# Kernel optimization log

Measured on AMD Instinct MI355X. Metric: run time of the kernel, lower is better.

## Reference

```python
import jax, jax.numpy as jnp
import numpy as np

N_NODES = 128   # input_series_dim (nodes per graph)
FEAT = 512      # input_series_length
HID = 512       # hidden_channels
OUT = 10        # output_dimension
BATCH = 512     # batch_size


def setup_inputs() -> dict:
    key = jax.random.key(0)
    ks = jax.random.split(key, 9)
    s = 0.02
    x = jax.random.normal(ks[0], (BATCH, N_NODES, FEAT), jnp.float32)
    # dense_to_sparse(ones(N_NODES, N_NODES)) -> fully connected incl. diagonal,
    # row-major order, covering only nodes 0..N_NODES-1 (faithful to source).
    r = jnp.repeat(jnp.arange(N_NODES, dtype=jnp.int32), N_NODES)
    c = jnp.tile(jnp.arange(N_NODES, dtype=jnp.int32), N_NODES)
    edge_index = jnp.stack([r, c])  # (2, N_NODES**2)
    batch = jnp.repeat(jnp.arange(BATCH, dtype=jnp.int32), N_NODES)  # (BATCH*N_NODES,)
    W1 = jax.random.normal(ks[1], (FEAT, HID), jnp.float32) * s
    b1 = jnp.zeros((HID,), jnp.float32)
    W2 = jax.random.normal(ks[2], (HID, HID), jnp.float32) * s
    b2 = jnp.zeros((HID,), jnp.float32)
    W3 = jax.random.normal(ks[3], (HID, HID), jnp.float32) * s
    b3 = jnp.zeros((HID,), jnp.float32)
    Wlin = jax.random.normal(ks[4], (HID, OUT), jnp.float32) * s
    blin = jnp.zeros((OUT,), jnp.float32)
    return {"x": x, "W1": W1, "b1": b1, "W2": W2, "b2": b2, "W3": W3,
            "b3": b3, "Wlin": Wlin, "blin": blin,
            "edge_index": edge_index, "batch": batch}


def gcn_conv(h, src, dst, W, b):
    # PyG GCNConv: linear transform, add self-loops for ALL N nodes, symmetric norm,
    # scatter-add aggregate at dst, add bias.
    N = h.shape[0]
    h = h @ W
    loop = jnp.arange(N, dtype=src.dtype)
    s = jnp.concatenate([src, loop])
    d = jnp.concatenate([dst, loop])
    deg = jax.ops.segment_sum(jnp.ones(s.shape[0], h.dtype), d, num_segments=N)
    dinv = jnp.where(deg > 0, jax.lax.rsqrt(deg), jnp.zeros((), h.dtype))
    norm = dinv[s] * dinv[d]                     # (E+N,)
    out = jax.ops.segment_sum(norm[:, None] * h[s], d, num_segments=N)
    return out + b


def reference(x, W1, b1, W2, b2, W3, b3, Wlin, blin, edge_index, batch):
    x = x.reshape(-1, x.shape[-1]).astype(jnp.float32)   # (B*N_NODES, FEAT)
    src, dst = edge_index[0], edge_index[1]
    h = jax.nn.relu(gcn_conv(x, src, dst, W1, b1))
    h = jax.nn.relu(gcn_conv(h, src, dst, W2, b2))
    h = gcn_conv(h, src, dst, W3, b3)                    # layers == 3 path
    B = BATCH
    sums = jax.ops.segment_sum(h, batch, num_segments=B)
    cnt = jax.ops.segment_sum(jnp.ones((h.shape[0],), h.dtype), batch, num_segments=B)
    pooled = sums / cnt[:, None]                         # global_mean_pool
    # dropout p=0.5 is identity in eval mode
    return pooled @ Wlin + blin                          # (BATCH, OUT)
```

## Files before the change

kernel.cpp:

```cpp
#include <hip/hip_runtime.h>
#include <hip/hip_bf16.h>


typedef __attribute__((ext_vector_type(8))) short short8;
typedef __attribute__((ext_vector_type(4))) float f32x4;
typedef __attribute__((ext_vector_type(2))) unsigned int uint2v;

#define AS_G __attribute__((address_space(1)))
#define AS_L __attribute__((address_space(3)))

__device__ __forceinline__ void gload_lds16(const void* g, void* l) {
  __builtin_amdgcn_global_load_lds((const AS_G void*)g, (AS_L void*)l, 16, 0, 0);
}

__device__ __forceinline__ unsigned int pack2_bf16(float a, float b) {
  unsigned int ua = __float_as_uint(a);
  unsigned int ub = __float_as_uint(b);
  ua += 0x7FFFu + ((ua >> 16) & 1u);
  ub += 0x7FFFu + ((ub >> 16) & 1u);
  return (ua >> 16) | (ub & 0xFFFF0000u);
}

__device__ __forceinline__ unsigned short bf16_rne(float a) {
  unsigned int ua = __float_as_uint(a);
  ua += 0x7FFFu + ((ua >> 16) & 1u);
  return (unsigned short)(ua >> 16);
}

__global__ __launch_bounds__(1024) void fused_gcn(
    const float* __restrict__ x,
    const __hip_bfloat16* __restrict__ W1t,
    const __hip_bfloat16* __restrict__ W2t,
    const float* __restrict__ b1,
    const float* __restrict__ b2,
    const float* __restrict__ Wf,
    const float* __restrict__ bfv,
    float* __restrict__ out)
{
  __shared__ __align__(16) __hip_bfloat16 smem[81920];

  const int t  = threadIdx.x;
  const int g  = blockIdx.x;
  const int wave = t >> 6;
  const int l    = t & 63;
  const int q    = l >> 4;
  const int r16  = l & 15;
  const int wm   = (wave & 1) * 64;
  const int wn   = (wave >> 1) * 64;

  const int arow = t >> 3;
  const int kq   = t & 7;
  const float* ga = x + ((size_t)g * 128 + arow) * 512 + kq * 4;
  const int awoff = arow * 32 + (((kq >> 1) ^ ((arow >> 1) & 3)) << 3) + (kq & 1) * 4;

  const int brow = t >> 2;
  const int bgc  = (t & 3) ^ ((brow >> 1) & 3);
  const size_t boff = (size_t)brow * 512 + bgc * 8;
  const __hip_bfloat16* g1b0 = W1t + boff;
  const __hip_bfloat16* g1b1 = g1b0 + (size_t)256 * 512;

  f32x4 acc[4][4];
#pragma unroll
  for (int i = 0; i < 4; ++i)
#pragma unroll
    for (int j = 0; j < 4; ++j)
      acc[i][j] = (f32x4)0.0f;

  {
    f32x4 a0 = *(const f32x4*)(const void*)ga;
    gload_lds16(g1b0, smem + 49152 + wave * 512);
    gload_lds16(g1b1, smem + 49152 + 8192 + wave * 512);
    uint2v w;
    w[0] = pack2_bf16(a0[0], a0[1]);
    w[1] = pack2_bf16(a0[2], a0[3]);
    *(uint2v*)(void*)(smem + awoff) = w;
  }
  for (int kt = 0; kt < 16; ++kt) {
    const int cur = kt & 1;
    const int nxt = cur ^ 1;
    __syncthreads();

    f32x4 aN;
    if (kt < 15) {
      const int ko = (kt + 1) * 32;
      aN = *(const f32x4*)(const void*)(ga + ko);
      gload_lds16(g1b0 + ko, smem + 49152 + nxt * 16384 + wave * 512);
      gload_lds16(g1b1 + ko, smem + 49152 + nxt * 16384 + 8192 + wave * 512);
    }

    short8 af[4], bfr[4];
#pragma unroll
    for (int i = 0; i < 4; ++i) {
      const int row = wm + i * 16 + r16;
      const int c   = (q ^ ((row >> 1) & 3)) << 3;
      af[i] = *(const short8*)(const void*)(smem + cur * 4096 + row * 32 + c);
    }
#pragma unroll
    for (int j = 0; j < 4; ++j) {
      const int row = wn + j * 16 + r16;
      const int c   = (q ^ ((row >> 1) & 3)) << 3;
      bfr[j] = *(const short8*)(const void*)(smem + 49152 + cur * 16384 + row * 32 + c);
    }
#pragma unroll
    for (int i = 0; i < 4; ++i)
#pragma unroll
      for (int j = 0; j < 4; ++j)
        acc[i][j] = __builtin_amdgcn_mfma_f32_16x16x32_bf16(af[i], bfr[j], acc[i][j], 0, 0, 0);

    if (kt < 15) {
      uint2v w;
      w[0] = pack2_bf16(aN[0], aN[1]);
      w[1] = pack2_bf16(aN[2], aN[3]);
      *(uint2v*)(void*)(smem + nxt * 4096 + awoff) = w;
    }
  }
  __syncthreads();

  const __hip_bfloat16* g2b0 = W2t + boff;
  const __hip_bfloat16* g2b1 = g2b0 + (size_t)256 * 512;
  gload_lds16(g2b0, smem + 65536 + wave * 512);

  float* redf = (float*)(smem + 73728);
  float* Sbuf = (float*)(smem + 75776);

  if (g == 0) {
    float sj[4];
#pragma unroll
    for (int j = 0; j < 4; ++j) {
      float a = 0.0f;
#pragma unroll
      for (int i = 0; i < 4; ++i)
#pragma unroll
        for (int r = 0; r < 4; ++r)
          a += acc[i][j][r];
      a += __shfl_xor(a, 16, 64);
      a += __shfl_xor(a, 32, 64);
      sj[j] = a;
    }
    if (q == 0) {
#pragma unroll
      for (int j = 0; j < 4; ++j) redf[wave * 64 + j * 16 + r16] = sj[j];
    }
    __syncthreads();
    if (t < 512)
      Sbuf[t] = redf[((t >> 6) * 2) * 64 + (t & 63)] +
                redf[((t >> 6) * 2 + 1) * 64 + (t & 63)];
    __syncthreads();
#pragma unroll
    for (int j = 0; j < 4; ++j) {
      const int col = wn + j * 16 + r16;
      const float bv = b1[col];
      const float Sv = Sbuf[col];
#pragma unroll
      for (int i = 0; i < 4; ++i)
#pragma unroll
        for (int r = 0; r < 4; ++r) {
          const int row = wm + i * 16 + q * 4 + r;
          const float v = fmaxf((Sv + acc[i][j][r]) * (1.0f / 129.0f) + bv, 0.0f);
          const float o = __shfl_xor(v, 1, 64);
          if ((r16 & 1) == 0) {
            const int sl = (col >> 3) ^ (row & 7);
            *(unsigned int*)(void*)(smem + row * 512 + sl * 8 + (col & 7)) = pack2_bf16(v, o);
          }
        }
    }
  } else {
#pragma unroll
    for (int j = 0; j < 4; ++j) {
      const int col = wn + j * 16 + r16;
      const float bv = b1[col];
#pragma unroll
      for (int i = 0; i < 4; ++i)
#pragma unroll
        for (int r = 0; r < 4; ++r) {
          const int row = wm + i * 16 + q * 4 + r;
          const float v = fmaxf(acc[i][j][r] + bv, 0.0f);
          const float o = __shfl_xor(v, 1, 64);
          if ((r16 & 1) == 0) {
            const int sl = (col >> 3) ^ (row & 7);
            *(unsigned int*)(void*)(smem + row * 512 + sl * 8 + (col & 7)) = pack2_bf16(v, o);
          }
        }
    }
  }

#pragma unroll
  for (int i = 0; i < 4; ++i)
#pragma unroll
    for (int j = 0; j < 4; ++j)
      acc[i][j] = (f32x4)0.0f;

  for (int kt = 0; kt < 16; ++kt) {
    __syncthreads();
    gload_lds16(g2b1 + kt * 32, smem + 73728 + wave * 512);
    if (wave < 8) {
      short8 af[4], bfr[4];
#pragma unroll
      for (int i = 0; i < 4; ++i) {
        const int row = wm + i * 16 + r16;
        const int sl  = (kt * 4 + q) ^ (row & 7);
        af[i] = *(const short8*)(const void*)(smem + row * 512 + sl * 8);
      }
#pragma unroll
      for (int j = 0; j < 4; ++j) {
        const int row = wn + j * 16 + r16;
        const int c   = (q ^ ((row >> 1) & 3)) << 3;
        bfr[j] = *(const short8*)(const void*)(smem + 65536 + row * 32 + c);
      }
      __builtin_amdgcn_s_setprio(1);
#pragma unroll
      for (int i = 0; i < 4; ++i)
#pragma unroll
        for (int j = 0; j < 4; ++j)
          acc[i][j] = __builtin_amdgcn_mfma_f32_16x16x32_bf16(af[i], bfr[j], acc[i][j], 0, 0, 0);
      __builtin_amdgcn_s_setprio(0);
    }
    __syncthreads();
    if (kt < 15)
      gload_lds16(g2b0 + (kt + 1) * 32, smem + 65536 + wave * 512);
    if (wave >= 8) {
      short8 af[4], bfr[4];
#pragma unroll
      for (int i = 0; i < 4; ++i) {
        const int row = wm + i * 16 + r16;
        const int sl  = (kt * 4 + q) ^ (row & 7);
        af[i] = *(const short8*)(const void*)(smem + row * 512 + sl * 8);
      }
#pragma unroll
      for (int j = 0; j < 4; ++j) {
        const int row = wn + j * 16 + r16;
        const int c   = (q ^ ((row >> 1) & 3)) << 3;
        bfr[j] = *(const short8*)(const void*)(smem + 65536 + row * 32 + c);
      }
      __builtin_amdgcn_s_setprio(1);
#pragma unroll
      for (int i = 0; i < 4; ++i)
#pragma unroll
        for (int j = 0; j < 4; ++j)
          acc[i][j] = __builtin_amdgcn_mfma_f32_16x16x32_bf16(af[i], bfr[j], acc[i][j], 0, 0, 0);
      __builtin_amdgcn_s_setprio(0);
    }
  }
  __syncthreads();

  float pj[4];
  if (g == 0) {
    float sj[4];
#pragma unroll
    for (int j = 0; j < 4; ++j) {
      float a = 0.0f;
#pragma unroll
      for (int i = 0; i < 4; ++i)
#pragma unroll
        for (int r = 0; r < 4; ++r)
          a += acc[i][j][r];
      a += __shfl_xor(a, 16, 64);
      a += __shfl_xor(a, 32, 64);
      sj[j] = a;
    }
    if (q == 0) {
#pragma unroll
      for (int j = 0; j < 4; ++j) redf[wave * 64 + j * 16 + r16] = sj[j];
    }
    __syncthreads();
    if (t < 512)
      Sbuf[t] = redf[((t >> 6) * 2) * 64 + (t & 63)] +
                redf[((t >> 6) * 2 + 1) * 64 + (t & 63)];
    __syncthreads();
#pragma unroll
    for (int j = 0; j < 4; ++j) {
      const float bv = b2[wn + j * 16 + r16];
      const float Sv = Sbuf[wn + j * 16 + r16];
      float a = 0.0f;
#pragma unroll
      for (int i = 0; i < 4; ++i)
#pragma unroll
        for (int r = 0; r < 4; ++r)
          a += fmaxf((Sv + acc[i][j][r]) * (1.0f / 129.0f) + bv, 0.0f);
      a += __shfl_xor(a, 16, 64);
      a += __shfl_xor(a, 32, 64);
      pj[j] = a;
    }
  } else {
#pragma unroll
    for (int j = 0; j < 4; ++j) {
      const float bv = b2[wn + j * 16 + r16];
      float a = 0.0f;
#pragma unroll
      for (int i = 0; i < 4; ++i)
#pragma unroll
        for (int r = 0; r < 4; ++r)
          a += fmaxf(acc[i][j][r] + bv, 0.0f);
      a += __shfl_xor(a, 16, 64);
      a += __shfl_xor(a, 32, 64);
      pj[j] = a;
    }
  }
  if (q == 0) {
#pragma unroll
    for (int j = 0; j < 4; ++j) redf[wave * 64 + j * 16 + r16] = pj[j];
  }
  __syncthreads();
  if (t < 512)
    Sbuf[t] =
        (redf[((t >> 6) * 2) * 64 + (t & 63)] +
         redf[((t >> 6) * 2 + 1) * 64 + (t & 63)]) * (1.0f / 128.0f);
  __syncthreads();

  if (wave < 10) {
    float s = 0.0f;
    for (int c = l; c < 512; c += 64) s += Sbuf[c] * Wf[c * 10 + wave];
#pragma unroll
    for (int off = 32; off; off >>= 1) s += __shfl_down(s, off, 64);
    if (l == 0) out[(size_t)g * 10 + wave] = s + bfv[wave];
  }
}

__global__ __launch_bounds__(1024) void prep(
    const float* __restrict__ W1, const float* __restrict__ W2,
    unsigned short* __restrict__ W1t, unsigned short* __restrict__ W2t,
    const float* __restrict__ W3, const float* __restrict__ Wlin,
    const float* __restrict__ b3, const float* __restrict__ blin,
    float* __restrict__ Wf, float* __restrict__ bfv) {
  const int b = blockIdx.x;
  if (b < 512) {
    __shared__ float tile[32][33];
    const int z  = b >> 8;
    const int by = (b >> 4) & 15;
    const int bx = b & 15;
    const float* W = z ? W2 : W1;
    unsigned short* Wt = z ? W2t : W1t;
    const int tx = threadIdx.x & 31;
    const int ty = threadIdx.x >> 5;
    tile[ty][tx] = W[(by * 32 + ty) * 512 + bx * 32 + tx];
    __syncthreads();
    Wt[(bx * 32 + ty) * 512 + by * 32 + tx] = bf16_rne(tile[tx][ty]);
  } else {
    const int c = b - 512;
    const int l = threadIdx.x;
    if (l < 64) {
      float acc[10];
#pragma unroll
      for (int o = 0; o < 10; ++o) acc[o] = 0.0f;
      for (int n = l; n < 512; n += 64) {
        const float wv = W3[c * 512 + n];
#pragma unroll
        for (int o = 0; o < 10; ++o) acc[o] += wv * Wlin[n * 10 + o];
      }
#pragma unroll
      for (int off = 32; off; off >>= 1)
#pragma unroll
        for (int o = 0; o < 10; ++o) acc[o] += __shfl_down(acc[o], off, 64);
      if (l == 0) {
#pragma unroll
        for (int o = 0; o < 10; ++o) Wf[c * 10 + o] = acc[o];
      }
      if (c < 10) {
        float s = 0.0f;
        for (int k = l; k < 512; k += 64) s += b3[k] * Wlin[k * 10 + c];
#pragma unroll
        for (int off = 32; off; off >>= 1) s += __shfl_down(s, off, 64);
        if (l == 0) bfv[c] = s + blin[c];
      }
    }
  }
}

extern "C" void kernel_launch(void* const* d_in, const int* in_sizes, int n_in,
                              void* d_out, int out_size, void* d_ws, size_t ws_size,
                              hipStream_t stream) {
  const float* x    = (const float*)d_in[0];
  const float* W1   = (const float*)d_in[1];
  const float* b1   = (const float*)d_in[2];
  const float* W2   = (const float*)d_in[3];
  const float* b2   = (const float*)d_in[4];
  const float* W3   = (const float*)d_in[5];
  const float* b3   = (const float*)d_in[6];
  const float* Wlin = (const float*)d_in[7];
  const float* blin = (const float*)d_in[8];
  float* out = (float*)d_out;

  char* ws = (char*)d_ws;
  unsigned short* W1t = (unsigned short*)ws;
  unsigned short* W2t = W1t + 512 * 512;
  float* Wf           = (float*)(W2t + 512 * 512);
  float* bfv          = Wf + 512 * 10;

  prep<<<1024, 1024, 0, stream>>>(W1, W2, W1t, W2t, W3, Wlin, b3, blin, Wf, bfv);

  fused_gcn<<<512, 1024, 0, stream>>>(
      x, (const __hip_bfloat16*)W1t, (const __hip_bfloat16*)W2t, b1, b2, Wf, bfv, out);
}
```

Baseline: 277.4 us.

## Split fused GCN kernel into two tiled GEMM kernels plus output kernel

Replaces the single per-graph fused kernel (1024 threads, large LDS) with two separate 128x256-tile bf16 MFMA GEMM kernels that write an intermediate H1 buffer in bf16 and pooled features P, followed by a small output projection kernel. The goal is higher occupancy (smaller blocks, 4 blocks per CU), double-buffered global-to-LDS loads, and an XCD-aware block remap. In exchange it adds a 64 MB bf16 round-trip through global memory and extra launches, and it falls back to the fused path when the workspace is too small. Graph 0's fully connected aggregation is folded into the epilogue, and the remaining graphs get only the self-loop.

New measurement: 320.8 us. 1.16x slower.

```diff
diff --git a/kernel.cpp b/kernel.cpp
--- a/kernel.cpp
+++ b/kernel.cpp
@@ -5,6 +5,7 @@
 typedef __attribute__((ext_vector_type(8))) short short8;
 typedef __attribute__((ext_vector_type(4))) float f32x4;
 typedef __attribute__((ext_vector_type(2))) unsigned int uint2v;
+typedef __attribute__((ext_vector_type(4))) unsigned int uint4v;
 
 #define AS_G __attribute__((address_space(1)))
 #define AS_L __attribute__((address_space(3)))
@@ -25,6 +26,341 @@
   unsigned int ua = __float_as_uint(a);
   ua += 0x7FFFu + ((ua >> 16) & 1u);
   return (unsigned short)(ua >> 16);
+}
+
+__global__ __launch_bounds__(512, 4) void gemm1(
+    const float* __restrict__ x,
+    const __hip_bfloat16* __restrict__ W1t,
+    const float* __restrict__ b1,
+    unsigned short* __restrict__ H1)
+{
+  __shared__ __align__(16) __hip_bfloat16 smem[26368];
+
+  const int t    = threadIdx.x;
+  const int orig = blockIdx.x;
+  const int wgid = (orig & 7) * 128 + (orig >> 3);
+  const int g    = wgid >> 1;
+  const int nb   = wgid & 1;
+
+  const int wave = t >> 6;
+  const int l    = t & 63;
+  const int q    = l >> 4;
+  const int r16  = l & 15;
+  const int wm   = (wave & 1) * 64;
+  const int wn   = (wave >> 1) * 64;
+
+  const int arow = t >> 2;
+  const int cc   = t & 3;
+  const float* gx = x + ((size_t)g * 128 + arow) * 512 + cc * 8;
+  const int awoff = arow * 32 + ((cc ^ ((arow >> 1) & 3)) << 3);
+
+  const int nrow0 = t >> 2;
+  const int nrow1 = (512 + t) >> 2;
+  const int slot  = t & 3;
+  const __hip_bfloat16* gb0 = W1t + (size_t)(nb * 256 + nrow0) * 512 +
+                              ((slot ^ ((nrow0 >> 1) & 3)) << 3);
+  const __hip_bfloat16* gb1 = W1t + (size_t)(nb * 256 + nrow1) * 512 +
+                              ((slot ^ ((nrow1 >> 1) & 3)) << 3);
+
+  f32x4 acc[4][4];
+#pragma unroll
+  for (int i = 0; i < 4; ++i)
+#pragma unroll
+    for (int j = 0; j < 4; ++j)
+      acc[i][j] = (f32x4)0.0f;
+
+  {
+    f32x4 a0 = *(const f32x4*)(const void*)gx;
+    f32x4 a1 = *(const f32x4*)(const void*)(gx + 4);
+    gload_lds16(gb0, smem + 8192 + wave * 512);
+    gload_lds16(gb1, smem + 8192 + 4096 + wave * 512);
+    uint4v w;
+    w[0] = pack2_bf16(a0[0], a0[1]);
+    w[1] = pack2_bf16(a0[2], a0[3]);
+    w[2] = pack2_bf16(a1[0], a1[1]);
+    w[3] = pack2_bf16(a1[2], a1[3]);
+    *(uint4v*)(void*)(smem + awoff) = w;
+  }
+
+  for (int kt = 0; kt < 16; ++kt) {
+    const int cur = kt & 1;
+    const int nxt = cur ^ 1;
+    __syncthreads();
+
+    f32x4 aN0, aN1;
+    if (kt < 15) {
+      const int ko = (kt + 1) * 32;
+      aN0 = *(const f32x4*)(const void*)(gx + ko);
+      aN1 = *(const f32x4*)(const void*)(gx + ko + 4);
+      gload_lds16(gb0 + ko, smem + 8192 + nxt * 8192 + wave * 512);
+      gload_lds16(gb1 + ko, smem + 8192 + nxt * 8192 + 4096 + wave * 512);
+    }
+
+    short8 af[4], bfr[4];
+#pragma unroll
+    for (int i = 0; i < 4; ++i) {
+      const int row = wm + i * 16 + r16;
+      const int c   = (q ^ ((row >> 1) & 3)) << 3;
+      af[i] = *(const short8*)(const void*)(smem + cur * 4096 + row * 32 + c);
+    }
+#pragma unroll
+    for (int j = 0; j < 4; ++j) {
+      const int row = wn + j * 16 + r16;
+      const int c   = (q ^ ((row >> 1) & 3)) << 3;
+      bfr[j] = *(const short8*)(const void*)(smem + 8192 + cur * 8192 + row * 32 + c);
+    }
+    __builtin_amdgcn_s_setprio(1);
+#pragma unroll
+    for (int i = 0; i < 4; ++i)
+#pragma unroll
+      for (int j = 0; j < 4; ++j)
+        acc[i][j] = __builtin_amdgcn_mfma_f32_16x16x32_bf16(af[i], bfr[j], acc[i][j], 0, 0, 0);
+    __builtin_amdgcn_s_setprio(0);
+
+    if (kt < 15) {
+      uint4v w;
+      w[0] = pack2_bf16(aN0[0], aN0[1]);
+      w[1] = pack2_bf16(aN0[2], aN0[3]);
+      w[2] = pack2_bf16(aN1[0], aN1[1]);
+      w[3] = pack2_bf16(aN1[2], aN1[3]);
+      *(uint4v*)(void*)(smem + nxt * 4096 + awoff) = w;
+    }
+  }
+
+  float* redf = (float*)(smem + 24576);
+  float* Sbuf = (float*)(smem + 25600);
+
+  if (g == 0) {
+    float sj[4];
+#pragma unroll
+    for (int j = 0; j < 4; ++j) {
+      float a = 0.0f;
+#pragma unroll
+      for (int i = 0; i < 4; ++i)
+#pragma unroll
+        for (int r = 0; r < 4; ++r)
+          a += acc[i][j][r];
+      a += __shfl_xor(a, 16, 64);
+      a += __shfl_xor(a, 32, 64);
+      sj[j] = a;
+    }
+    __syncthreads();
+    if (q == 0) {
+#pragma unroll
+      for (int j = 0; j < 4; ++j) redf[wave * 64 + j * 16 + r16] = sj[j];
+    }
+    __syncthreads();
+    if (t < 256)
+      Sbuf[t] = redf[(2 * (t >> 6)) * 64 + (t & 63)] +
+                redf[(2 * (t >> 6) + 1) * 64 + (t & 63)];
+    __syncthreads();
+#pragma unroll
+    for (int j = 0; j < 4; ++j) {
+      const int col = wn + j * 16 + r16;
+      const float bv = b1[nb * 256 + col];
+      const float Sv = Sbuf[col];
+#pragma unroll
+      for (int i = 0; i < 4; ++i)
+#pragma unroll
+        for (int r = 0; r < 4; ++r) {
+          const int row = wm + i * 16 + q * 4 + r;
+          const float v = fmaxf((Sv + acc[i][j][r]) * (1.0f / 129.0f) + bv, 0.0f);
+          const float o = __shfl_xor(v, 1, 64);
+          if ((r16 & 1) == 0)
+            *(unsigned int*)(void*)(H1 + (size_t)(g * 128 + row) * 512 + nb * 256 + col) =
+                pack2_bf16(v, o);
+        }
+    }
+  } else {
+#pragma unroll
+    for (int j = 0; j < 4; ++j) {
+      const int col = wn + j * 16 + r16;
+      const float bv = b1[nb * 256 + col];
+#pragma unroll
+      for (int i = 0; i < 4; ++i)
+#pragma unroll
+        for (int r = 0; r < 4; ++r) {
+          const int row = wm + i * 16 + q * 4 + r;
+          const float v = fmaxf(acc[i][j][r] + bv, 0.0f);
+          const float o = __shfl_xor(v, 1, 64);
+          if ((r16 & 1) == 0)
+            *(unsigned int*)(void*)(H1 + (size_t)(g * 128 + row) * 512 + nb * 256 + col) =
+                pack2_bf16(v, o);
+        }
+    }
+  }
+}
+
+__global__ __launch_bounds__(512, 4) void gemm2(
+    const unsigned short* __restrict__ H1,
+    const __hip_bfloat16* __restrict__ W2t,
+    const float* __restrict__ b2,
+    float* __restrict__ P)
+{
+  __shared__ __align__(16) __hip_bfloat16 smem[26368];
+
+  const int t    = threadIdx.x;
+  const int orig = blockIdx.x;
+  const int wgid = (orig & 7) * 128 + (orig >> 3);
+  const int g    = wgid >> 1;
+  const int nb   = wgid & 1;
+
+  const int wave = t >> 6;
+  const int l    = t & 63;
+  const int q    = l >> 4;
+  const int r16  = l & 15;
+  const int wm   = (wave & 1) * 64;
+  const int wn   = (wave >> 1) * 64;
+
+  const int arow = t >> 2;
+  const int slot = t & 3;
+  const unsigned short* gaA = H1 + (size_t)(g * 128 + arow) * 512 +
+                              ((slot ^ ((arow >> 1) & 3)) << 3);
+  const int nrow0 = t >> 2;
+  const int nrow1 = (512 + t) >> 2;
+  const __hip_bfloat16* gb0 = W2t + (size_t)(nb * 256 + nrow0) * 512 +
+                              ((slot ^ ((nrow0 >> 1) & 3)) << 3);
+  const __hip_bfloat16* gb1 = W2t + (size_t)(nb * 256 + nrow1) * 512 +
+                              ((slot ^ ((nrow1 >> 1) & 3)) << 3);
+
+  f32x4 acc[4][4];
+#pragma unroll
+  for (int i = 0; i < 4; ++i)
+#pragma unroll
+    for (int j = 0; j < 4; ++j)
+      acc[i][j] = (f32x4)0.0f;
+
+  gload_lds16(gaA, smem + wave * 512);
+  gload_lds16(gb0, smem + 8192 + wave * 512);
+  gload_lds16(gb1, smem + 8192 + 4096 + wave * 512);
+
+  for (int kt = 0; kt < 16; ++kt) {
+    const int cur = kt & 1;
+    const int nxt = cur ^ 1;
+    __syncthreads();
+
+    if (kt < 15) {
+      const int ko = (kt + 1) * 32;
+      gload_lds16(gaA + ko, smem + nxt * 4096 + wave * 512);
+      gload_lds16(gb0 + ko, smem + 8192 + nxt * 8192 + wave * 512);
+      gload_lds16(gb1 + ko, smem + 8192 + nxt * 8192 + 4096 + wave * 512);
+    }
+
+    short8 af[4], bfr[4];
+#pragma unroll
+    for (int i = 0; i < 4; ++i) {
+      const int row = wm + i * 16 + r16;
+      const int c   = (q ^ ((row >> 1) & 3)) << 3;
+      af[i] = *(const short8*)(const void*)(smem + cur * 4096 + row * 32 + c);
+    }
+#pragma unroll
+    for (int j = 0; j < 4; ++j) {
+      const int row = wn + j * 16 + r16;
+      const int c   = (q ^ ((row >> 1) & 3)) << 3;
+      bfr[j] = *(const short8*)(const void*)(smem + 8192 + cur * 8192 + row * 32 + c);
+    }
+    __builtin_amdgcn_s_setprio(1);
+#pragma unroll
+    for (int i = 0; i < 4; ++i)
+#pragma unroll
+      for (int j = 0; j < 4; ++j)
+        acc[i][j] = __builtin_amdgcn_mfma_f32_16x16x32_bf16(af[i], bfr[j], acc[i][j], 0, 0, 0);
+    __builtin_amdgcn_s_setprio(0);
+  }
+
+  float* redf = (float*)(smem + 24576);
+  float* Sbuf = (float*)(smem + 25600);
+
+  float pj[4];
+  if (g == 0) {
+    float sj[4];
+#pragma unroll
+    for (int j = 0; j < 4; ++j) {
+      float a = 0.0f;
+#pragma unroll
+      for (int i = 0; i < 4; ++i)
+#pragma unroll
+        for (int r = 0; r < 4; ++r)
+          a += acc[i][j][r];
+      a += __shfl_xor(a, 16, 64);
+      a += __shfl_xor(a, 32, 64);
+      sj[j] = a;
+    }
+    __syncthreads();
+    if (q == 0) {
+#pragma unroll
+      for (int j = 0; j < 4; ++j) redf[wave * 64 + j * 16 + r16] = sj[j];
+    }
+    __syncthreads();
+    if (t < 256)
+      Sbuf[t] = redf[(2 * (t >> 6)) * 64 + (t & 63)] +
+                redf[(2 * (t >> 6) + 1) * 64 + (t & 63)];
+    __syncthreads();
+#pragma unroll
+    for (int j = 0; j < 4; ++j) {
+      const int col = wn + j * 16 + r16;
+      const float bv = b2[nb * 256 + col];
+      const float Sv = Sbuf[col];
+      float a = 0.0f;
+#pragma unroll
+      for (int i = 0; i < 4; ++i)
+#pragma unroll
+        for (int r = 0; r < 4; ++r)
+          a += fmaxf((Sv + acc[i][j][r]) * (1.0f / 129.0f) + bv, 0.0f);
+      a += __shfl_xor(a, 16, 64);
+      a += __shfl_xor(a, 32, 64);
+      pj[j] = a;
+    }
+    __syncthreads();
+  } else {
+#pragma unroll
+    for (int j = 0; j < 4; ++j) {
+      const float bv = b2[nb * 256 + wn + j * 16 + r16];
+      float a = 0.0f;
+#pragma unroll
+      for (int i = 0; i < 4; ++i)
+#pragma unroll
+        for (int r = 0; r < 4; ++r)
+          a += fmaxf(acc[i][j][r] + bv, 0.0f);
+      a += __shfl_xor(a, 16, 64);
+      a += __shfl_xor(a, 32, 64);
+      pj[j] = a;
+    }
+    __syncthreads();
+  }
+  if (q == 0) {
+#pragma unroll
+    for (int j = 0; j < 4; ++j) redf[wave * 64 + j * 16 + r16] = pj[j];
+  }
+  __syncthreads();
+  if (t < 256)
+    P[(size_t)g * 512 + nb * 256 + t] =
+        (redf[(2 * (t >> 6)) * 64 + (t & 63)] +
+         redf[(2 * (t >> 6) + 1) * 64 + (t & 63)]) * (1.0f / 128.0f);
+}
+
+__global__ void final_out(const float* __restrict__ P,
+                          const float* __restrict__ Wf,
+                          const float* __restrict__ bfv,
+                          float* __restrict__ out) {
+  const int m = blockIdx.x;
+  const int l = threadIdx.x;
+  float acc[10];
+#pragma unroll
+  for (int o = 0; o < 10; ++o) acc[o] = 0.0f;
+  for (int c = l; c < 512; c += 64) {
+    const float p = P[m * 512 + c];
+#pragma unroll
+    for (int o = 0; o < 10; ++o) acc[o] += p * Wf[c * 10 + o];
+  }
+#pragma unroll
+  for (int off = 32; off; off >>= 1)
+#pragma unroll
+    for (int o = 0; o < 10; ++o) acc[o] += __shfl_down(acc[o], off, 64);
+  if (l == 0) {
+#pragma unroll
+    for (int o = 0; o < 10; ++o) out[m * 10 + o] = acc[o] + bfv[o];
+  }
 }
 
 __global__ __launch_bounds__(1024) void fused_gcn(
@@ -385,9 +721,23 @@
   unsigned short* W2t = W1t + 512 * 512;
   float* Wf           = (float*)(W2t + 512 * 512);
   float* bfv          = Wf + 512 * 10;
+  float* P            = bfv + 16;
+  unsigned short* H1  = (unsigned short*)(P + 512 * 512);
+
+  const size_t need = (size_t)(W2t + 512 * 512 - W1t) * 2 +
+                      (512 * 10 + 16 + 512 * 512) * 4 +
+                      (size_t)65536 * 512 * 2;
 
   prep<<<1024, 1024, 0, stream>>>(W1, W2, W1t, W2t, W3, Wlin, b3, blin, Wf, bfv);
 
-  fused_gcn<<<512, 1024, 0, stream>>>(
-      x, (const __hip_bfloat16*)W1t, (const __hip_bfloat16*)W2t, b1, b2, Wf, bfv, out);
-}
+  if (ws_size >= need) {
+    gemm1<<<1024, 512, 0, stream>>>(
+        x, (const __hip_bfloat16*)W1t, b1, H1);
+    gemm2<<<1024, 512, 0, stream>>>(
+        H1, (const __hip_bfloat16*)W2t, b2, P);
+    final_out<<<512, 64, 0, stream>>>(P, Wf, bfv, out);
+  } else {
+    fused_gcn<<<512, 1024, 0, stream>>>(
+        x, (const __hip_bfloat16*)W1t, (const __hip_bfloat16*)W2t, b1, b2, Wf, bfv, out);
+  }
+}
```
